# Optimization experiments

Hardware: AMD Instinct MI355X
Metric: run time of the kernel (lower is better)

Reference implementation:

```python
import jax, jax.numpy as jnp
import numpy as np
import itertools

# LeViT-style Attention config (matches init_kwargs)
DIM = 256
KD = 32          # key_dim
H = 8            # num_heads
AR = 4           # attn_ratio
RES = 14
N = RES * RES    # 196 tokens
D = AR * KD      # per-head value dim = 128
DH = D * H       # 1024
NHKD = KD * H    # 256
HID = DH + 2 * NHKD  # 1536 = qkv width
EPS = 1e-5
SCALE = KD ** -0.5
BATCH = 256


def _bias_idxs():
    # Same construction as the torch module: index into table of unique abs offsets.
    points = list(itertools.product(range(RES), range(RES)))
    offs = {}
    idxs = []
    for p1 in points:
        for p2 in points:
            o = (abs(p1[0] - p2[0]), abs(p1[1] - p2[1]))
            if o not in offs:
                offs[o] = len(offs)
            idxs.append(offs[o])
    return np.asarray(idxs, dtype=np.int32).reshape(N, N), len(offs)


def _bn(x, g, b):
    # BatchNorm1d in training mode over the flattened (B*N, F) batch dim.
    mu = x.mean(axis=0)
    var = jnp.var(x, axis=0)  # biased, as torch BN uses for normalization
    return (x - mu) * jax.lax.rsqrt(var + EPS) * g + b


def setup_inputs() -> dict:
    key = jax.random.key(0)
    ks = jax.random.split(key, 8)
    idxs_np, n_off = _bias_idxs()  # n_off == 196 for RES=14
    x = jax.random.normal(ks[0], (BATCH, N, DIM), dtype=jnp.float32)
    Wqkv = jax.random.normal(ks[1], (HID, DIM), dtype=jnp.float32) * 0.02
    g1 = 1.0 + 0.1 * jax.random.normal(ks[2], (HID,), dtype=jnp.float32)
    b1 = 0.1 * jax.random.normal(ks[3], (HID,), dtype=jnp.float32)
    # init is zeros in the module; use small randn so the bias path is exercised
    bias_table = 0.1 * jax.random.normal(ks[4], (H, n_off), dtype=jnp.float32)
    Wproj = jax.random.normal(ks[5], (DIM, DH), dtype=jnp.float32) * 0.02
    # bn_weight_init=0 in module; use nonzero so output/grads are nontrivial
    g2 = 1.0 + 0.1 * jax.random.normal(ks[6], (DIM,), dtype=jnp.float32)
    b2 = 0.1 * jax.random.normal(ks[7], (DIM,), dtype=jnp.float32)
    return {
        "x": x, "Wqkv": Wqkv, "g1": g1, "b1": b1,
        "bias_table": bias_table, "Wproj": Wproj, "g2": g2, "b2": b2,
        "idxs": jnp.asarray(idxs_np),
    }


def reference(x, Wqkv, g1, b1, bias_table, Wproj, g2, b2, idxs):
    B, Ntok, C = x.shape
    # qkv = Linear_BN(x): bias-free linear then BN over flattened (B*N, HID)
    h = jnp.einsum('bnc,hc->bnh', x, Wqkv)
    h = _bn(h.reshape(B * Ntok, HID), g1, b1).reshape(B, Ntok, H, -1)
    q = h[..., :KD].transpose(0, 2, 1, 3)            # (B,H,N,KD)
    k = h[..., KD:2 * KD].transpose(0, 2, 1, 3)      # (B,H,N,KD)
    v = h[..., 2 * KD:].transpose(0, 2, 1, 3)        # (B,H,N,D)
    bias = bias_table[:, idxs]                       # (H,N,N) relative-position bias gather
    attn = jnp.einsum('bhnd,bhmd->bhnm', q, k) * SCALE + bias
    attn = jax.nn.softmax(attn, axis=-1)
    o = jnp.einsum('bhnm,bhmd->bhnd', attn, v)
    o = o.transpose(0, 2, 1, 3).reshape(B, Ntok, DH)
    # proj = Hardswish -> Linear_BN(dh, dim)
    o = o * jnp.clip(o + 3.0, 0.0, 6.0) / 6.0
    o = jnp.einsum('bnd,cd->bnc', o, Wproj)
    o = _bn(o.reshape(B * Ntok, C), g2, b2).reshape(B, Ntok, C)
    return o
```

## Files before the change

### kernel.cpp

```cpp
#include <hip/hip_runtime.h>

typedef _Float16 f16;
typedef __attribute__((ext_vector_type(8))) _Float16 half8;
typedef __attribute__((ext_vector_type(4))) _Float16 half4;
typedef __attribute__((ext_vector_type(4))) float   f4;

#define NTOK   196
#define MROWS  50176
#define HIDN   1536
#define HPC    192
#define DHD    1024
#define EPSV   1e-5f
#define SCALEV 0.17677669529663687f

#define GLD16(gp, lp) __builtin_amdgcn_global_load_lds( \
    (const __attribute__((address_space(1))) unsigned int*)(gp), \
    (__attribute__((address_space(3))) unsigned int*)(lp), 16, 0, 0)

__device__ inline int swz8(int row) { return (((row & 7) ^ ((row >> 3) & 7))) * 8; }

__global__ void cvt_f32_f16(const float* __restrict__ src, f16* __restrict__ dst, int n4)
{
    int i = blockIdx.x * blockDim.x + threadIdx.x;
    if (i < n4) {
        float4 v = *(const float4*)&src[i * 4];
        half4 h = { (f16)v.x, (f16)v.y, (f16)v.z, (f16)v.w };
        *(half4*)&dst[i * 4] = h;
    }
}

__global__ void build_bias(const float* __restrict__ bt, const int* __restrict__ idxs,
                           f16* __restrict__ bf)
{
    int i = blockIdx.x * 256 + threadIdx.x;
    if (i >= 8 * 208 * 224) return;
    int k = i % 224, q = (i / 224) % 208, h = i / (224 * 208);
    float v = -30000.f;
    if (q < NTOK && k < NTOK) v = bt[h * NTOK + idxs[q * NTOK + k]];
    bf[i] = (f16)v;
}

__global__ __launch_bounds__(256) void gemm1_qkv(
    const f16* __restrict__ A, const f16* __restrict__ B,
    f16* __restrict__ C, float* __restrict__ gsum, float* __restrict__ gsq)
{
    const int K = 256, ldc = HIDN;
    __shared__ f16 As[128 * 32];
    __shared__ f16 Bs[128 * 32];
    __shared__ float ssum[128], ssq[128];

    const int t = threadIdx.x;
    const int m0 = blockIdx.x * 128, n0 = blockIdx.y * 128;
    const int wid = t >> 6, lane = t & 63, quad = lane >> 4, lm = lane & 15;
    const int wm = (wid >> 1) * 64, wn = (wid & 1) * 64;

    const int lr = lane >> 2, lc = (lane & 3) * 8;
    f16* As0 = &As[(wid * 2 + 0) * 512];
    f16* As1 = &As[(wid * 2 + 1) * 512];
    f16* Bs0 = &Bs[(wid * 2 + 0) * 512];
    f16* Bs1 = &Bs[(wid * 2 + 1) * 512];
    const f16* Ab = A + (long)(m0 + wid * 32 + lr) * K + lc;
    const f16* Bb = B + (long)(n0 + wid * 32 + lr) * K + lc;

    f4 acc[4][4] = {};

    for (int k0 = 0; k0 < K; k0 += 32) {
        GLD16(Ab + k0,          As0);
        GLD16(Ab + 16 * K + k0, As1);
        GLD16(Bb + k0,          Bs0);
        GLD16(Bb + 16 * K + k0, Bs1);
        __syncthreads();
        half8 a[4], b[4];
        #pragma unroll
        for (int i = 0; i < 4; ++i) a[i] = *(const half8*)&As[(wm + i*16 + lm) * 32 + quad * 8];
        #pragma unroll
        for (int j = 0; j < 4; ++j) b[j] = *(const half8*)&Bs[(wn + j*16 + lm) * 32 + quad * 8];
        #pragma unroll
        for (int i = 0; i < 4; ++i)
            #pragma unroll
            for (int j = 0; j < 4; ++j)
                acc[i][j] = __builtin_amdgcn_mfma_f32_16x16x32_f16(a[i], b[j], acc[i][j], 0, 0, 0);
        __syncthreads();
    }

    if (t < 128) { ssum[t] = 0.f; ssq[t] = 0.f; }
    __syncthreads();

    #pragma unroll
    for (int j = 0; j < 4; ++j) {
        int nl = wn + j*16 + lm;
        float psum = 0.f, psq = 0.f;
        #pragma unroll
        for (int i = 0; i < 4; ++i) {
            #pragma unroll
            for (int r = 0; r < 4; ++r) {
                int ml = wm + i*16 + quad*4 + r;
                float v = acc[i][j][r];
                f16 uh = (f16)v;
                float vb = (float)uh;
                C[(long)(m0 + ml) * ldc + n0 + nl] = uh;
                psum += vb; psq += vb * vb;
            }
        }
        atomicAdd(&ssum[nl], psum);
        atomicAdd(&ssq[nl], psq);
    }
    __syncthreads();
    if (t < 128) {
        atomicAdd(&gsum[n0 + t], ssum[t]);
        atomicAdd(&gsq[n0 + t],  ssq[t]);
    }
}

__global__ __launch_bounds__(256) void gemm2_proj(
    const f16* __restrict__ A, const f16* __restrict__ B,
    float* __restrict__ C, float* __restrict__ gsum, float* __restrict__ gsq)
{
    const int K = 1024, ldc = 256;
    __shared__ f16 As[128 * 32];
    __shared__ f16 Bs[128 * 32];
    __shared__ float ssum[128], ssq[128];

    const int t = threadIdx.x;
    const int m0 = blockIdx.x * 128, n0 = blockIdx.y * 128;
    const int wid = t >> 6, lane = t & 63, quad = lane >> 4, lm = lane & 15;
    const int wm = (wid >> 1) * 64, wn = (wid & 1) * 64;

    const int lr = lane >> 2, lc = (lane & 3) * 8;
    f16* As0 = &As[(wid * 2 + 0) * 512];
    f16* As1 = &As[(wid * 2 + 1) * 512];
    f16* Bs0 = &Bs[(wid * 2 + 0) * 512];
    f16* Bs1 = &Bs[(wid * 2 + 1) * 512];
    const f16* Ab = A + (long)(m0 + wid * 32 + lr) * K + lc;
    const f16* Bb = B + (long)(n0 + wid * 32 + lr) * K + lc;

    f4 acc[4][4] = {};

    for (int k0 = 0; k0 < K; k0 += 32) {
        GLD16(Ab + k0,          As0);
        GLD16(Ab + 16 * K + k0, As1);
        GLD16(Bb + k0,          Bs0);
        GLD16(Bb + 16 * K + k0, Bs1);
        __syncthreads();
        half8 a[4], b[4];
        #pragma unroll
        for (int i = 0; i < 4; ++i) a[i] = *(const half8*)&As[(wm + i*16 + lm) * 32 + quad * 8];
        #pragma unroll
        for (int j = 0; j < 4; ++j) b[j] = *(const half8*)&Bs[(wn + j*16 + lm) * 32 + quad * 8];
        #pragma unroll
        for (int i = 0; i < 4; ++i)
            #pragma unroll
            for (int j = 0; j < 4; ++j)
                acc[i][j] = __builtin_amdgcn_mfma_f32_16x16x32_f16(a[i], b[j], acc[i][j], 0, 0, 0);
        __syncthreads();
    }

    if (t < 128) { ssum[t] = 0.f; ssq[t] = 0.f; }
    __syncthreads();

    #pragma unroll
    for (int j = 0; j < 4; ++j) {
        int nl = wn + j*16 + lm;
        float psum = 0.f, psq = 0.f;
        #pragma unroll
        for (int i = 0; i < 4; ++i) {
            #pragma unroll
            for (int r = 0; r < 4; ++r) {
                int ml = wm + i*16 + quad*4 + r;
                float v = acc[i][j][r];
                C[(long)(m0 + ml) * ldc + n0 + nl] = v;
                psum += v; psq += v * v;
            }
        }
        atomicAdd(&ssum[nl], psum);
        atomicAdd(&ssq[nl], psq);
    }
    __syncthreads();
    if (t < 128) {
        atomicAdd(&gsum[n0 + t], ssum[t]);
        atomicAdd(&gsq[n0 + t],  ssq[t]);
    }
}

__global__ void bn_fin(const float* __restrict__ gsum, const float* __restrict__ gsq,
                       const float* __restrict__ g, const float* __restrict__ b,
                       float* __restrict__ a_out, float* __restrict__ s_out, int nch)
{
    int c = blockIdx.x * blockDim.x + threadIdx.x;
    if (c >= nch) return;
    float inv  = 1.f / (float)MROWS;
    float mean = gsum[c] * inv;
    float var  = gsq[c] * inv - mean * mean;
    float a    = g[c] * rsqrtf(var + EPSV);
    a_out[c] = a;
    s_out[c] = b[c] - mean * a;
}

__global__ __launch_bounds__(512) void attn_kernel(
    const f16* __restrict__ hbuf, const float* __restrict__ a1, const float* __restrict__ s1,
    const f16* __restrict__ bf, f16* __restrict__ obuf)
{
    __shared__ f16   qs[208][32];
    __shared__ f16   ks[208][32];
    __shared__ f16   vT[128][256];
    __shared__ f16   ps[8][16][256];
    __shared__ float af[192], sf[192];

    const int t  = threadIdx.x;
    const int bb = blockIdx.x >> 3;
    const int hh = blockIdx.x & 7;
    const int wid = t >> 6, lane = t & 63, quad = lane >> 4, lm = lane & 15;

    if (t < 192) { af[t] = a1[hh * HPC + t]; sf[t] = s1[hh * HPC + t]; }
    half8 z8 = {};
    for (int i = t; i < 4096; i += 512) *(half8*)&vT[i >> 5][(i & 31) * 8] = z8;
    for (int i = t; i < 4096; i += 512) *(half8*)&ps[i >> 9][(i >> 5) & 15][(i & 31) * 8] = z8;
    for (int i = t; i < 12 * 32; i += 512) { qs[196 + (i >> 5)][i & 31] = (f16)0.f;
                                             ks[196 + (i >> 5)][i & 31] = (f16)0.f; }
    __syncthreads();

    {
        int t8 = t & 7;
        for (int rr = t >> 3; rr < NTOK; rr += 64) {
            const f16* hrow = hbuf + (long)(bb * NTOK + rr) * HIDN + hh * HPC;
            int sr = swz8(rr);
            #pragma unroll
            for (int cc = 0; cc < 3; ++cc) {
                int cb = (t8 + cc * 8) * 8;
                half8 raw = *(const half8*)(hrow + cb);
                f16 ov[8];
                #pragma unroll
                for (int e = 0; e < 8; ++e)
                    ov[e] = (f16)((float)raw[e] * af[cb + e] + sf[cb + e]);
                if (cb < 32) {
                    #pragma unroll
                    for (int e = 0; e < 8; ++e) qs[rr][(cb + e + sr) & 31] = ov[e];
                } else if (cb < 64) {
                    #pragma unroll
                    for (int e = 0; e < 8; ++e) ks[rr][(cb - 32 + e + sr) & 31] = ov[e];
                } else {
                    #pragma unroll
                    for (int e = 0; e < 8; ++e) {
                        int c = cb - 64 + e;
                        vT[c][(rr + swz8(c)) & 255] = ov[e];
                    }
                }
            }
        }
    }
    __syncthreads();

    const int nmt = (wid + 8 < 13) ? 2 : 1;
    half8 ap[2][7];
    const f16* bfh = bf + hh * 208 * 224;

    for (int pass = 0; pass < nmt; ++pass) {
        const int mt = wid + pass * 8;
        int qrowA = mt * 16 + lm;
        half8 aq = *(const half8*)&qs[qrowA][(quad * 8 + swz8(qrowA)) & 31];
        f4 sreg[13];
        #pragma unroll
        for (int nt = 0; nt < 13; ++nt) {
            int krow = nt * 16 + lm;
            half8 bk = *(const half8*)&ks[krow][(quad * 8 + swz8(krow)) & 31];
            f4 z = {};
            sreg[nt] = __builtin_amdgcn_mfma_f32_16x16x32_f16(aq, bk, z, 0, 0, 0);
        }
        #pragma unroll
        for (int nt = 0; nt < 13; ++nt) {
            int kc = nt * 16 + lm;
            #pragma unroll
            for (int r = 0; r < 4; ++r) {
                int qrow = mt * 16 + quad * 4 + r;
                float bias_v = (float)bfh[qrow * 224 + kc];
                sreg[nt][r] = sreg[nt][r] * SCALEV + bias_v;
            }
        }
        float rinv[4];
        #pragma unroll
        for (int r = 0; r < 4; ++r) {
            float m = sreg[0][r];
            #pragma unroll
            for (int nt = 1; nt < 13; ++nt) m = fmaxf(m, sreg[nt][r]);
            #pragma unroll
            for (int d = 1; d < 16; d <<= 1) m = fmaxf(m, __shfl_xor(m, d));
            float s = 0.f;
            #pragma unroll
            for (int nt = 0; nt < 13; ++nt) {
                float e = __expf(sreg[nt][r] - m);
                sreg[nt][r] = e;
                s += e;
            }
            #pragma unroll
            for (int d = 1; d < 16; d <<= 1) s += __shfl_xor(s, d);
            rinv[r] = 1.f / s;
        }
        #pragma unroll
        for (int nt = 0; nt < 13; ++nt)
            #pragma unroll
            for (int r = 0; r < 4; ++r) {
                int q = quad * 4 + r;
                ps[wid][q][(nt * 16 + lm + swz8(q)) & 255] = (f16)(sreg[nt][r] * rinv[r]);
            }
        #pragma unroll
        for (int k7 = 0; k7 < 7; ++k7)
            ap[pass][k7] = *(const half8*)&ps[wid][lm][(k7 * 32 + quad * 8 + swz8(lm)) & 255];
    }

    #pragma unroll
    for (int ct = 0; ct < 8; ++ct) {
        int c = ct * 16 + lm;
        int sc = swz8(c);
        f4 oa0 = {}, oa1 = {};
        #pragma unroll
        for (int k7 = 0; k7 < 7; ++k7) {
            half8 bv = *(const half8*)&vT[c][(k7 * 32 + quad * 8 + sc) & 255];
            oa0 = __builtin_amdgcn_mfma_f32_16x16x32_f16(ap[0][k7], bv, oa0, 0, 0, 0);
            if (nmt == 2)
                oa1 = __builtin_amdgcn_mfma_f32_16x16x32_f16(ap[1][k7], bv, oa1, 0, 0, 0);
        }
        #pragma unroll
        for (int r = 0; r < 4; ++r) {
            int qrow = wid * 16 + quad * 4 + r;
            if (qrow < 196) {
                float v  = oa0[r];
                float hs = v * fminf(fmaxf(v + 3.f, 0.f), 6.f) * (1.f / 6.f);
                obuf[(long)(bb * NTOK + qrow) * DHD + hh * 128 + c] = (f16)hs;
            }
        }
        if (nmt == 2) {
            #pragma unroll
            for (int r = 0; r < 4; ++r) {
                int qrow = (wid + 8) * 16 + quad * 4 + r;
                if (qrow < 196) {
                    float v  = oa1[r];
                    float hs = v * fminf(fmaxf(v + 3.f, 0.f), 6.f) * (1.f / 6.f);
                    obuf[(long)(bb * NTOK + qrow) * DHD + hh * 128 + c] = (f16)hs;
                }
            }
        }
    }
}

__global__ __launch_bounds__(256) void bn_apply(
    float* __restrict__ out, const float* __restrict__ a2, const float* __restrict__ s2)
{
    __shared__ float aL[256], sL[256];
    int t = threadIdx.x;
    aL[t] = a2[t]; sL[t] = s2[t];
    __syncthreads();
    long total = (long)MROWS * 256 / 4;
    for (long i = (long)blockIdx.x * 256 + t; i < total; i += (long)gridDim.x * 256) {
        float4 v = *(float4*)&out[i * 4];
        int cb = (int)((i * 4) & 255);
        v.x = v.x * aL[cb + 0] + sL[cb + 0];
        v.y = v.y * aL[cb + 1] + sL[cb + 1];
        v.z = v.z * aL[cb + 2] + sL[cb + 2];
        v.w = v.w * aL[cb + 3] + sL[cb + 3];
        *(float4*)&out[i * 4] = v;
    }
}

extern "C" void kernel_launch(void* const* d_in, const int* in_sizes, int n_in,
                              void* d_out, int out_size, void* d_ws, size_t ws_size,
                              hipStream_t stream)
{
    (void)in_sizes; (void)n_in; (void)out_size; (void)ws_size;
    const float* x          = (const float*)d_in[0];
    const float* Wqkv       = (const float*)d_in[1];
    const float* g1         = (const float*)d_in[2];
    const float* b1         = (const float*)d_in[3];
    const float* bias_table = (const float*)d_in[4];
    const float* Wproj      = (const float*)d_in[5];
    const float* g2         = (const float*)d_in[6];
    const float* b2         = (const float*)d_in[7];
    const int*   idxs       = (const int*)d_in[8];
    float*       out        = (float*)d_out;

    char* ws = (char*)d_ws;
    f16* hbuf = (f16*)ws;
    f16* obuf = (f16*)(ws + 154140672LL);
    f16* xh   = (f16*)(ws + 154140672LL);
    f16* wqh  = (f16*)(ws + 154140672LL + 25690112LL);
    f16* wph  = (f16*)ws;
    float* stats = (float*)(ws + 256901120LL);
    float* gsum1 = stats;            float* gsq1 = stats + 1536;
    float* gsum2 = stats + 3072;     float* gsq2 = stats + 3328;
    float* a1 = stats + 3584;        float* s1 = a1 + 1536;
    float* a2 = s1 + 1536;           float* s2 = a2 + 256;
    f16* bias_full = (f16*)(ws + 256901120LL + 65536LL);

    hipMemsetAsync(stats, 0, 3584 * sizeof(float), stream);

    cvt_f32_f16<<<12544, 256, 0, stream>>>(x, xh, 3211264);
    cvt_f32_f16<<<384,   256, 0, stream>>>(Wqkv, wqh, 98304);
    build_bias<<<1456, 256, 0, stream>>>(bias_table, idxs, bias_full);

    gemm1_qkv<<<dim3(392, 12), 256, 0, stream>>>(xh, wqh, hbuf, gsum1, gsq1);
    bn_fin<<<6, 256, 0, stream>>>(gsum1, gsq1, g1, b1, a1, s1, 1536);

    attn_kernel<<<2048, 512, 0, stream>>>(hbuf, a1, s1, bias_full, obuf);

    cvt_f32_f16<<<256, 256, 0, stream>>>(Wproj, wph, 65536);

    gemm2_proj<<<dim3(392, 2), 256, 0, stream>>>(obuf, wph, out, gsum2, gsq2);
    bn_fin<<<1, 256, 0, stream>>>(gsum2, gsq2, g2, b2, a2, s2, 256);

    bn_apply<<<1024, 256, 0, stream>>>(out, a2, s2);
}
```

Measured before the change: 474.9 us.

## Keep attention probabilities in registers via transposed QK^T and pre-normalized Q/K

The QK^T MFMA is now computed with keys as the A operand and queries as the B operand. Its accumulator layout then feeds the PV 16x16x16 MFMA directly from registers, so the per-wave probability staging buffer in shared memory and its round trip are gone. BN scaling of Q and K moves to a separate elementwise kernel that rewrites hbuf in place, letting the attention kernel load Q/K fragments straight from global memory. LDS drops to only the transposed V tile, and launch bounds now request higher occupancy. The cost is an extra read/write pass over the Q/K columns, uncoalesced per-fragment global loads, and padded key rows that read past each batch's 196 tokens.

Result: slower. 501.0 us (+5.5%).

```diff
diff --git a/kernel.cpp b/kernel.cpp
--- a/kernel.cpp
+++ b/kernel.cpp
@@ -196,146 +196,172 @@
     s_out[c] = b[c] - mean * a;
 }
 
-__global__ __launch_bounds__(512) void attn_kernel(
+__global__ __launch_bounds__(256) void bn1_qk(
+    f16* __restrict__ h, const float* __restrict__ a1, const float* __restrict__ s1)
+{
+    int i = blockIdx.x * 256 + threadIdx.x;
+    int row = i >> 6, j = i & 63;
+    int hh = j >> 3, c8 = (j & 7) * 8;
+    size_t off = (size_t)row * HIDN + hh * HPC + c8;
+    int ci = hh * HPC + c8;
+    half8 v = *(half8*)(h + off);
+    float4 a0 = *(const float4*)&a1[ci], a4 = *(const float4*)&a1[ci + 4];
+    float4 s0 = *(const float4*)&s1[ci], s4 = *(const float4*)&s1[ci + 4];
+    half8 o;
+    o[0] = (f16)((float)v[0] * a0.x + s0.x);
+    o[1] = (f16)((float)v[1] * a0.y + s0.y);
+    o[2] = (f16)((float)v[2] * a0.z + s0.z);
+    o[3] = (f16)((float)v[3] * a0.w + s0.w);
+    o[4] = (f16)((float)v[4] * a4.x + s4.x);
+    o[5] = (f16)((float)v[5] * a4.y + s4.y);
+    o[6] = (f16)((float)v[6] * a4.z + s4.z);
+    o[7] = (f16)((float)v[7] * a4.w + s4.w);
+    *(half8*)(h + off) = o;
+}
+
+__global__ __launch_bounds__(512, 4) void attn_kernel(
     const f16* __restrict__ hbuf, const float* __restrict__ a1, const float* __restrict__ s1,
     const f16* __restrict__ bf, f16* __restrict__ obuf)
 {
-    __shared__ f16   qs[208][32];
-    __shared__ f16   ks[208][32];
-    __shared__ f16   vT[128][256];
-    __shared__ f16   ps[8][16][256];
-    __shared__ float af[192], sf[192];
+    __shared__ f16   vT[128][208];
+    __shared__ float af[128], sf[128];
 
     const int t  = threadIdx.x;
     const int bb = blockIdx.x >> 3;
     const int hh = blockIdx.x & 7;
     const int wid = t >> 6, lane = t & 63, quad = lane >> 4, lm = lane & 15;
 
-    if (t < 192) { af[t] = a1[hh * HPC + t]; sf[t] = s1[hh * HPC + t]; }
-    half8 z8 = {};
-    for (int i = t; i < 4096; i += 512) *(half8*)&vT[i >> 5][(i & 31) * 8] = z8;
-    for (int i = t; i < 4096; i += 512) *(half8*)&ps[i >> 9][(i >> 5) & 15][(i & 31) * 8] = z8;
-    for (int i = t; i < 12 * 32; i += 512) { qs[196 + (i >> 5)][i & 31] = (f16)0.f;
-                                             ks[196 + (i >> 5)][i & 31] = (f16)0.f; }
+    if (t < 128) { af[t] = a1[hh * HPC + 64 + t]; sf[t] = s1[hh * HPC + 64 + t]; }
+    for (int i = t; i < 1536; i += 512) {
+        int c = i & 127, kc = 196 + (i >> 7);
+        int p = kc + swz8(c); if (p >= 208) p -= 208;
+        vT[c][p] = (f16)0.f;
+    }
     __syncthreads();
 
     {
-        int t8 = t & 7;
-        for (int rr = t >> 3; rr < NTOK; rr += 64) {
-            const f16* hrow = hbuf + (long)(bb * NTOK + rr) * HIDN + hh * HPC;
-            int sr = swz8(rr);
-            #pragma unroll
-            for (int cc = 0; cc < 3; ++cc) {
-                int cb = (t8 + cc * 8) * 8;
-                half8 raw = *(const half8*)(hrow + cb);
-                f16 ov[8];
-                #pragma unroll
-                for (int e = 0; e < 8; ++e)
-                    ov[e] = (f16)((float)raw[e] * af[cb + e] + sf[cb + e]);
-                if (cb < 32) {
-                    #pragma unroll
-                    for (int e = 0; e < 8; ++e) qs[rr][(cb + e + sr) & 31] = ov[e];
-                } else if (cb < 64) {
-                    #pragma unroll
-                    for (int e = 0; e < 8; ++e) ks[rr][(cb - 32 + e + sr) & 31] = ov[e];
-                } else {
-                    #pragma unroll
-                    for (int e = 0; e < 8; ++e) {
-                        int c = cb - 64 + e;
-                        vT[c][(rr + swz8(c)) & 255] = ov[e];
-                    }
-                }
+        int tc = t & 15;
+        for (int rr = t >> 4; rr < NTOK; rr += 32) {
+            const f16* hrow = hbuf + (size_t)(bb * NTOK + rr) * HIDN + hh * HPC + 64;
+            half8 raw = *(const half8*)(hrow + tc * 8);
+            #pragma unroll
+            for (int e = 0; e < 8; ++e) {
+                int c = tc * 8 + e;
+                int p = rr + swz8(c); if (p >= 208) p -= 208;
+                vT[c][p] = (f16)((float)raw[e] * af[c] + sf[c]);
             }
         }
     }
     __syncthreads();
 
-    const int nmt = (wid + 8 < 13) ? 2 : 1;
-    half8 ap[2][7];
+    const f16* kb  = hbuf + (size_t)(bb * NTOK) * HIDN + hh * HPC + 32;
+    const f16* qb  = hbuf + (size_t)(bb * NTOK) * HIDN + hh * HPC;
     const f16* bfh = bf + hh * 208 * 224;
 
-    for (int pass = 0; pass < nmt; ++pass) {
-        const int mt = wid + pass * 8;
-        int qrowA = mt * 16 + lm;
-        half8 aq = *(const half8*)&qs[qrowA][(quad * 8 + swz8(qrowA)) & 31];
-        f4 sreg[13];
+    const int mt0 = wid, mt1 = wid + 8;
+    const int nmt = (mt1 < 13) ? 2 : 1;
+
+    half8 bq0 = *(const half8*)(qb + (size_t)(mt0 * 16 + lm) * HIDN + quad * 8);
+    half8 bq1 = bq0;
+    if (nmt == 2) bq1 = *(const half8*)(qb + (size_t)(mt1 * 16 + lm) * HIDN + quad * 8);
+
+    f4 sA[13], sB[13];
+    #pragma unroll
+    for (int nt = 0; nt < 13; ++nt) {
+        half8 ak = *(const half8*)(kb + (size_t)(nt * 16 + lm) * HIDN + quad * 8);
+        f4 z = {};
+        sA[nt] = __builtin_amdgcn_mfma_f32_16x16x32_f16(ak, bq0, z, 0, 0, 0);
+        if (nmt == 2) sB[nt] = __builtin_amdgcn_mfma_f32_16x16x32_f16(ak, bq1, z, 0, 0, 0);
+    }
+
+    half4 ap0[13], ap1[13];
+    {
         #pragma unroll
         for (int nt = 0; nt < 13; ++nt) {
-            int krow = nt * 16 + lm;
-            half8 bk = *(const half8*)&ks[krow][(quad * 8 + swz8(krow)) & 31];
-            f4 z = {};
-            sreg[nt] = __builtin_amdgcn_mfma_f32_16x16x32_f16(aq, bk, z, 0, 0, 0);
-        }
+            half4 bv = *(const half4*)(bfh + (mt0 * 16 + lm) * 224 + nt * 16 + quad * 4);
+            #pragma unroll
+            for (int r = 0; r < 4; ++r) sA[nt][r] = sA[nt][r] * SCALEV + (float)bv[r];
+        }
+        float mx = sA[0][0];
+        #pragma unroll
+        for (int nt = 0; nt < 13; ++nt)
+            #pragma unroll
+            for (int r = 0; r < 4; ++r) mx = fmaxf(mx, sA[nt][r]);
+        mx = fmaxf(mx, __shfl_xor(mx, 16));
+        mx = fmaxf(mx, __shfl_xor(mx, 32));
+        float sum = 0.f;
+        #pragma unroll
+        for (int nt = 0; nt < 13; ++nt)
+            #pragma unroll
+            for (int r = 0; r < 4; ++r) { float e = __expf(sA[nt][r] - mx); sA[nt][r] = e; sum += e; }
+        sum += __shfl_xor(sum, 16);
+        sum += __shfl_xor(sum, 32);
+        float ri = 1.f / sum;
         #pragma unroll
         for (int nt = 0; nt < 13; ++nt) {
-            int kc = nt * 16 + lm;
-            #pragma unroll
-            for (int r = 0; r < 4; ++r) {
-                int qrow = mt * 16 + quad * 4 + r;
-                float bias_v = (float)bfh[qrow * 224 + kc];
-                sreg[nt][r] = sreg[nt][r] * SCALEV + bias_v;
-            }
-        }
-        float rinv[4];
-        #pragma unroll
-        for (int r = 0; r < 4; ++r) {
-            float m = sreg[0][r];
-            #pragma unroll
-            for (int nt = 1; nt < 13; ++nt) m = fmaxf(m, sreg[nt][r]);
-            #pragma unroll
-            for (int d = 1; d < 16; d <<= 1) m = fmaxf(m, __shfl_xor(m, d));
-            float s = 0.f;
-            #pragma unroll
-            for (int nt = 0; nt < 13; ++nt) {
-                float e = __expf(sreg[nt][r] - m);
-                sreg[nt][r] = e;
-                s += e;
-            }
-            #pragma unroll
-            for (int d = 1; d < 16; d <<= 1) s += __shfl_xor(s, d);
-            rinv[r] = 1.f / s;
-        }
+            half4 p = { (f16)(sA[nt][0] * ri), (f16)(sA[nt][1] * ri),
+                        (f16)(sA[nt][2] * ri), (f16)(sA[nt][3] * ri) };
+            ap0[nt] = p;
+        }
+    }
+    if (nmt == 2) {
+        #pragma unroll
+        for (int nt = 0; nt < 13; ++nt) {
+            half4 bv = *(const half4*)(bfh + (mt1 * 16 + lm) * 224 + nt * 16 + quad * 4);
+            #pragma unroll
+            for (int r = 0; r < 4; ++r) sB[nt][r] = sB[nt][r] * SCALEV + (float)bv[r];
+        }
+        float mx = sB[0][0];
         #pragma unroll
         for (int nt = 0; nt < 13; ++nt)
             #pragma unroll
-            for (int r = 0; r < 4; ++r) {
-                int q = quad * 4 + r;
-                ps[wid][q][(nt * 16 + lm + swz8(q)) & 255] = (f16)(sreg[nt][r] * rinv[r]);
-            }
-        #pragma unroll
-        for (int k7 = 0; k7 < 7; ++k7)
-            ap[pass][k7] = *(const half8*)&ps[wid][lm][(k7 * 32 + quad * 8 + swz8(lm)) & 255];
+            for (int r = 0; r < 4; ++r) mx = fmaxf(mx, sB[nt][r]);
+        mx = fmaxf(mx, __shfl_xor(mx, 16));
+        mx = fmaxf(mx, __shfl_xor(mx, 32));
+        float sum = 0.f;
+        #pragma unroll
+        for (int nt = 0; nt < 13; ++nt)
+            #pragma unroll
+            for (int r = 0; r < 4; ++r) { float e = __expf(sB[nt][r] - mx); sB[nt][r] = e; sum += e; }
+        sum += __shfl_xor(sum, 16);
+        sum += __shfl_xor(sum, 32);
+        float ri = 1.f / sum;
+        #pragma unroll
+        for (int nt = 0; nt < 13; ++nt) {
+            half4 p = { (f16)(sB[nt][0] * ri), (f16)(sB[nt][1] * ri),
+                        (f16)(sB[nt][2] * ri), (f16)(sB[nt][3] * ri) };
+            ap1[nt] = p;
+        }
     }
 
     #pragma unroll
     for (int ct = 0; ct < 8; ++ct) {
         int c = ct * 16 + lm;
         int sc = swz8(c);
-        f4 oa0 = {}, oa1 = {};
-        #pragma unroll
-        for (int k7 = 0; k7 < 7; ++k7) {
-            half8 bv = *(const half8*)&vT[c][(k7 * 32 + quad * 8 + sc) & 255];
-            oa0 = __builtin_amdgcn_mfma_f32_16x16x32_f16(ap[0][k7], bv, oa0, 0, 0, 0);
+        f4 o0 = {}, o1 = {};
+        #pragma unroll
+        for (int kt = 0; kt < 13; ++kt) {
+            int p = kt * 16 + quad * 4 + sc; if (p >= 208) p -= 208;
+            half4 bv = *(const half4*)&vT[c][p];
+            o0 = __builtin_amdgcn_mfma_f32_16x16x16f16(ap0[kt], bv, o0, 0, 0, 0);
             if (nmt == 2)
-                oa1 = __builtin_amdgcn_mfma_f32_16x16x32_f16(ap[1][k7], bv, oa1, 0, 0, 0);
+                o1 = __builtin_amdgcn_mfma_f32_16x16x16f16(ap1[kt], bv, o1, 0, 0, 0);
         }
         #pragma unroll
         for (int r = 0; r < 4; ++r) {
-            int qrow = wid * 16 + quad * 4 + r;
-            if (qrow < 196) {
-                float v  = oa0[r];
-                float hs = v * fminf(fmaxf(v + 3.f, 0.f), 6.f) * (1.f / 6.f);
-                obuf[(long)(bb * NTOK + qrow) * DHD + hh * 128 + c] = (f16)hs;
-            }
+            int q0 = mt0 * 16 + quad * 4 + r;
+            float v = o0[r];
+            float hs = v * fminf(fmaxf(v + 3.f, 0.f), 6.f) * (1.f / 6.f);
+            obuf[(size_t)(bb * NTOK + q0) * DHD + hh * 128 + c] = (f16)hs;
         }
         if (nmt == 2) {
             #pragma unroll
             for (int r = 0; r < 4; ++r) {
-                int qrow = (wid + 8) * 16 + quad * 4 + r;
-                if (qrow < 196) {
-                    float v  = oa1[r];
+                int q1 = mt1 * 16 + quad * 4 + r;
+                if (q1 < NTOK) {
+                    float v = o1[r];
                     float hs = v * fminf(fmaxf(v + 3.f, 0.f), 6.f) * (1.f / 6.f);
-                    obuf[(long)(bb * NTOK + qrow) * DHD + hh * 128 + c] = (f16)hs;
+                    obuf[(size_t)(bb * NTOK + q1) * DHD + hh * 128 + c] = (f16)hs;
                 }
             }
         }
@@ -398,6 +424,7 @@
 
     gemm1_qkv<<<dim3(392, 12), 256, 0, stream>>>(xh, wqh, hbuf, gsum1, gsq1);
     bn_fin<<<6, 256, 0, stream>>>(gsum1, gsq1, g1, b1, a1, s1, 1536);
+    bn1_qk<<<12544, 256, 0, stream>>>(hbuf, a1, s1);
 
     attn_kernel<<<2048, 512, 0, stream>>>(hbuf, a1, s1, bias_full, obuf);
 
```
